# Optimization experiments

Hardware: AMD Instinct MI355X
Metric: run time of the kernel (lower is better)

## Reference

```python
import jax, jax.numpy as jnp
import numpy as np
from jax import lax

EPS = 1e-5

def _conv1d(x, w, b):
    # x: [B,C,L], w: [O,I,K], valid padding, stride 1
    y = lax.conv_general_dilated(x, w, window_strides=(1,), padding='VALID',
                                 dimension_numbers=('NCH', 'OIH', 'NCH'))
    return y + b[None, :, None]

def setup_inputs() -> dict:
    key = jax.random.key(0)
    ks = jax.random.split(key, 7)
    B, L, C = 16, 4096, 512
    x = jax.random.normal(ks[0], (B, L, C), dtype=jnp.float32)
    fan3 = 1.0 / np.sqrt(C * 3)
    fan1 = 1.0 / np.sqrt(C * 1)
    w_down = jax.random.uniform(ks[1], (C, C, 3), jnp.float32, -fan3, fan3)
    b_down = jax.random.uniform(ks[2], (C,), jnp.float32, -fan3, fan3)
    w_pad = jax.random.uniform(ks[3], (C, C, 1), jnp.float32, -fan1, fan1)
    b_pad = jax.random.uniform(ks[4], (C,), jnp.float32, -fan1, fan1)
    gamma = jnp.ones((C,), jnp.float32)
    beta = jnp.zeros((C,), jnp.float32)
    return {"x": x, "w_down": w_down, "b_down": b_down,
            "w_pad": w_pad, "b_pad": b_pad, "gamma": gamma, "beta": beta}

def reference(x, w_down, b_down, w_pad, b_pad, gamma, beta):
    # d == 2 branch of ConvLayer
    B, L, C = x.shape

    def branch(xs):  # xs: [B, L//2, C]
        xt = jnp.transpose(xs, (0, 2, 1))                 # [B,C,L/2]
        p1 = _conv1d(xt, w_down, b_down)                  # [B,C,L/2-2]
        p2 = _conv1d(xt[:, :, :2], w_pad, b_pad)          # [B,C,2]
        return jnp.concatenate([p1, p2], axis=2)          # [B,C,L/2]

    x1_p = branch(x[:, 0::2, :])
    x2_p = branch(x[:, 1::2, :])
    # interleave: even positions from x1_p, odd from x2_p
    x_p = jnp.stack([x1_p, x2_p], axis=3).reshape(B, C, L)

    # BatchNorm1d in training mode: batch stats over (batch, length)
    mean = jnp.mean(x_p, axis=(0, 2), keepdims=True)
    var = jnp.var(x_p, axis=(0, 2), keepdims=True)
    xn = (x_p - mean) * lax.rsqrt(var + EPS)
    xn = xn * gamma[None, :, None] + beta[None, :, None]

    y = jax.nn.elu(xn)                                    # dropout = identity (eval)
    y = y + jnp.transpose(x, (0, 2, 1))                   # residual [B,C,L]

    # MaxPool1d(kernel=3, stride=2, padding=1)
    yp = jnp.pad(y, ((0, 0), (0, 0), (1, 1)), constant_values=-jnp.inf)
    pooled = lax.reduce_window(yp, -jnp.inf, lax.max, (1, 1, 3), (1, 1, 2), 'VALID')
    return jnp.transpose(pooled, (0, 2, 1))               # [B, L//2, C]
```

## Files before the change

kernel.cpp:

```cpp
#include <hip/hip_runtime.h>
#include <hip/hip_bf16.h>
#include <math.h>

typedef __bf16 bf16;
typedef __bf16 bf16x8 __attribute__((ext_vector_type(8)));
typedef float floatx4 __attribute__((ext_vector_type(4)));

#define GAS __attribute__((address_space(1)))
#define LAS __attribute__((address_space(3)))

static constexpr int B_ = 16, L_ = 4096, C_ = 512;
static constexpr int M_ = B_ * L_;
static constexpr int K_ = 3 * C_;

__global__ void prep_w(const float* __restrict__ x,
                       const float* __restrict__ wd, bf16* __restrict__ wr,
                       const float* __restrict__ wp, const float* __restrict__ bp,
                       bf16* __restrict__ xp, float* __restrict__ sums) {
    __shared__ float xrow[C_];
    if (blockIdx.x < 512) {
        for (int u = blockIdx.x; u < 3072; u += 512) {
            int idx = u * 256 + threadIdx.x;
            int o   = idx / K_;
            int rem = idx - o * K_;
            int kk  = rem >> 9;
            int i   = rem & 511;
            wr[idx] = (bf16)wd[o * K_ + i * 3 + kk];
        }
    } else {
        const int bid = blockIdx.x - 512;
        const int b = bid >> 2;
        const int j = bid & 3;
        for (int i = threadIdx.x; i < C_; i += 256)
            xrow[i] = x[(size_t)(b * L_ + j) * C_ + i];
        __syncthreads();
        for (int c = threadIdx.x; c < C_; c += 256) {
            const float* w = wp + (size_t)c * C_;
            float acc = 0.f;
#pragma unroll 4
            for (int i = 0; i < C_; i += 4) {
                floatx4 wv = *(const floatx4*)(w + i);
#pragma unroll
                for (int u = 0; u < 4; ++u) acc += wv[u] * xrow[i + u];
            }
            const float v = acc + bp[c];
            xp[(size_t)(b * L_ + 4092 + j) * C_ + c] = (bf16)v;
            atomicAdd(&sums[c], v);
            atomicAdd(&sums[C_ + c], v * v);
        }
    }
}

__global__ __launch_bounds__(512, 2) void gemm_conv(
    const float* __restrict__ xf, const bf16* __restrict__ wr,
    const float* __restrict__ bd, bf16* __restrict__ xp,
    bf16* __restrict__ xb, float* __restrict__ sums)
{
    __shared__ bf16 As[2 * 256 * 64];
    __shared__ bf16 Bs[2 * 256 * 64];

    const int tid = threadIdx.x;
    const int u   = blockIdx.x;
    const int mb  = (u & 7) + 8 * (u >> 4);
    const int nb  = (u >> 3) & 1;
    const int m0  = mb * 256;
    const int n0  = nb * 256;

    const int wave = tid >> 6;
    const int lane = tid & 63;
    const int wm = wave & 1;
    const int wn = wave >> 1;
    const int tm = lane & 15;
    const int quad = lane >> 4;

    floatx4 acc[2][4][2][2];
#pragma unroll
    for (int a = 0; a < 2; ++a)
#pragma unroll
        for (int b = 0; b < 4; ++b)
#pragma unroll
            for (int c = 0; c < 2; ++c)
#pragma unroll
                for (int d = 0; d < 2; ++d) acc[a][b][c][d] = floatx4{0.f, 0.f, 0.f, 0.f};

    const int r0  = tid >> 3;
    const int c0s = (tid & 7) ^ (r0 & 7);

    auto issueA = [&](int ts, floatx4 (&va)[8]) {
        if (ts >= 24) return;
        const int kk = ts >> 3, i0 = (ts & 7) << 6;
#pragma unroll
        for (int eta = 0; eta < 2; ++eta) {
            int sr0 = m0 + eta * 128 + r0 + 2 * kk;      if (sr0 > M_ - 1) sr0 = M_ - 1;
            int sr1 = m0 + eta * 128 + r0 + 64 + 2 * kk; if (sr1 > M_ - 1) sr1 = M_ - 1;
            const float* p0 = xf + (size_t)sr0 * C_ + i0 + c0s * 8;
            const float* p1 = xf + (size_t)sr1 * C_ + i0 + c0s * 8;
            va[eta * 4 + 0] = *(const floatx4*)(p0);
            va[eta * 4 + 1] = *(const floatx4*)(p0 + 4);
            va[eta * 4 + 2] = *(const floatx4*)(p1);
            va[eta * 4 + 3] = *(const floatx4*)(p1 + 4);
        }
    };
    auto writeA = [&](int ts, const floatx4 (&va)[8]) {
        if (ts >= 24) return;
#pragma unroll
        for (int eta = 0; eta < 2; ++eta) {
            bf16* dst = As + (ts & 1) * 16384 + eta * 8192 + tid * 8;
            bf16x8 v0, v1;
#pragma unroll
            for (int j = 0; j < 4; ++j) {
                v0[j] = (bf16)va[eta * 4 + 0][j]; v0[4 + j] = (bf16)va[eta * 4 + 1][j];
                v1[j] = (bf16)va[eta * 4 + 2][j]; v1[4 + j] = (bf16)va[eta * 4 + 3][j];
            }
            *(bf16x8*)dst = v0;
            *(bf16x8*)(dst + 4096) = v1;
            if (nb == 0 && ts < 8) {
                const int i0 = ts << 6;
                const int sr0 = m0 + eta * 128 + r0;
                *(bf16x8*)(xb + (size_t)sr0 * C_ + i0 + c0s * 8) = v0;
                *(bf16x8*)(xb + (size_t)(sr0 + 64) * C_ + i0 + c0s * 8) = v1;
            }
        }
    };
    auto stageB = [&](int t, int eta) {
        if (t >= 24) return;
        const int kk = t >> 3, i0 = (t & 7) << 6;
        bf16* dst = Bs + (t & 1) * 16384 + eta * 8192 + tid * 8;
        const bf16* s0 = wr + (size_t)(n0 + eta * 128 + r0) * K_ + kk * C_ + i0 + c0s * 8;
        __builtin_amdgcn_global_load_lds((const GAS void*)s0, (LAS void*)dst, 16, 0, 0);
        __builtin_amdgcn_global_load_lds((const GAS void*)(s0 + (size_t)64 * K_),
                                         (LAS void*)(dst + 4096), 16, 0, 0);
    };

    const int xo0 = (quad ^ (tm & 7)) << 3;
    const int xo1 = ((4 + quad) ^ (tm & 7)) << 3;

    bf16x8 af[4][2];
    bf16x8 bfr[2][2][2];

    {
        floatx4 va0[8], va1[8];
        issueA(0, va0);
        issueA(1, va1);
        stageB(0, 0); stageB(0, 1); stageB(1, 0); stageB(1, 1);
        asm volatile("s_waitcnt vmcnt(8)" ::: "memory");
        writeA(0, va0);
        writeA(1, va1);
        asm volatile("s_waitcnt vmcnt(12) lgkmcnt(0)" ::: "memory");
        asm volatile("s_barrier" ::: "memory");
    }
#pragma unroll
    for (int mi = 0; mi < 4; ++mi) {
        const bf16* p = As + (wm * 64 + mi * 16 + tm) * 64;
        af[mi][0] = *(const bf16x8*)(p + xo0);
        af[mi][1] = *(const bf16x8*)(p + xo1);
    }
#pragma unroll
    for (int ni = 0; ni < 2; ++ni) {
        const bf16* p = Bs + (wn * 32 + ni * 16 + tm) * 64;
        bfr[0][ni][0] = *(const bf16x8*)(p + xo0);
        bfr[0][ni][1] = *(const bf16x8*)(p + xo1);
    }

#pragma unroll 2
    for (int t = 0; t < 24; ++t) {
        const bf16* Ab  = As + (t & 1) * 16384;
        const bf16* Bb  = Bs + (t & 1) * 16384;
        const bf16* AbN = As + ((t + 1) & 1) * 16384;
        const bf16* BbN = Bs + ((t + 1) & 1) * 16384;
        floatx4 va[8];

        asm volatile("s_waitcnt lgkmcnt(0)" ::: "memory");
        __builtin_amdgcn_sched_barrier(0);
        __builtin_amdgcn_s_setprio(1);
#pragma unroll
        for (int kh = 0; kh < 2; ++kh)
#pragma unroll
            for (int mi = 0; mi < 4; ++mi)
#pragma unroll
                for (int ni = 0; ni < 2; ++ni)
                    acc[0][mi][0][ni] = __builtin_amdgcn_mfma_f32_16x16x32_bf16(
                        af[mi][kh], bfr[0][ni][kh], acc[0][mi][0][ni], 0, 0, 0);
        __builtin_amdgcn_s_setprio(0);
#pragma unroll
        for (int ni = 0; ni < 2; ++ni) {
            const bf16* p = Bb + (128 + wn * 32 + ni * 16 + tm) * 64;
            bfr[1][ni][0] = *(const bf16x8*)(p + xo0);
            bfr[1][ni][1] = *(const bf16x8*)(p + xo1);
        }
        asm volatile("s_barrier" ::: "memory");

        asm volatile("s_waitcnt lgkmcnt(0)" ::: "memory");
        __builtin_amdgcn_sched_barrier(0);
        __builtin_amdgcn_s_setprio(1);
#pragma unroll
        for (int kh = 0; kh < 2; ++kh)
#pragma unroll
            for (int mi = 0; mi < 4; ++mi)
#pragma unroll
                for (int ni = 0; ni < 2; ++ni)
                    acc[0][mi][1][ni] = __builtin_amdgcn_mfma_f32_16x16x32_bf16(
                        af[mi][kh], bfr[1][ni][kh], acc[0][mi][1][ni], 0, 0, 0);
        __builtin_amdgcn_s_setprio(0);
#pragma unroll
        for (int mi = 0; mi < 4; ++mi) {
            const bf16* p = Ab + (128 + wm * 64 + mi * 16 + tm) * 64;
            af[mi][0] = *(const bf16x8*)(p + xo0);
            af[mi][1] = *(const bf16x8*)(p + xo1);
        }
        issueA(t + 2, va);
        stageB(t + 2, 0);
        asm volatile("s_barrier" ::: "memory");

        asm volatile("s_waitcnt lgkmcnt(0)" ::: "memory");
        __builtin_amdgcn_sched_barrier(0);
        __builtin_amdgcn_s_setprio(1);
#pragma unroll
        for (int kh = 0; kh < 2; ++kh)
#pragma unroll
            for (int mi = 0; mi < 4; ++mi)
#pragma unroll
                for (int ni = 0; ni < 2; ++ni)
                    acc[1][mi][1][ni] = __builtin_amdgcn_mfma_f32_16x16x32_bf16(
                        af[mi][kh], bfr[1][ni][kh], acc[1][mi][1][ni], 0, 0, 0);
        __builtin_amdgcn_s_setprio(0);
        stageB(t + 2, 1);
        asm volatile("s_barrier" ::: "memory");

        if (t < 22)       { asm volatile("s_waitcnt vmcnt(4)" ::: "memory"); }
        else if (t == 22) { asm volatile("s_waitcnt vmcnt(0)" ::: "memory"); }
        writeA(t + 2, va);
        asm volatile("s_barrier" ::: "memory");
        __builtin_amdgcn_s_setprio(1);
#pragma unroll
        for (int kh = 0; kh < 2; ++kh)
#pragma unroll
            for (int mi = 0; mi < 4; ++mi)
#pragma unroll
                for (int ni = 0; ni < 2; ++ni)
                    acc[1][mi][0][ni] = __builtin_amdgcn_mfma_f32_16x16x32_bf16(
                        af[mi][kh], bfr[0][ni][kh], acc[1][mi][0][ni], 0, 0, 0);
        __builtin_amdgcn_s_setprio(0);
        if (t < 23) {
#pragma unroll
            for (int mi = 0; mi < 4; ++mi) {
                const bf16* p = AbN + (wm * 64 + mi * 16 + tm) * 64;
                af[mi][0] = *(const bf16x8*)(p + xo0);
                af[mi][1] = *(const bf16x8*)(p + xo1);
            }
#pragma unroll
            for (int ni = 0; ni < 2; ++ni) {
                const bf16* p = BbN + (wn * 32 + ni * 16 + tm) * 64;
                bfr[0][ni][0] = *(const bf16x8*)(p + xo0);
                bfr[0][ni][1] = *(const bf16x8*)(p + xo1);
            }
        }
        asm volatile("s_barrier" ::: "memory");
    }

    float bias[2][2], s[2][2], q[2][2];
#pragma unroll
    for (int nh = 0; nh < 2; ++nh)
#pragma unroll
        for (int ni = 0; ni < 2; ++ni) {
            bias[nh][ni] = bd[n0 + nh * 128 + wn * 32 + ni * 16 + tm];
            s[nh][ni] = 0.f; q[nh][ni] = 0.f;
        }

#pragma unroll
    for (int mh = 0; mh < 2; ++mh)
#pragma unroll
        for (int mi = 0; mi < 4; ++mi)
#pragma unroll
            for (int r = 0; r < 4; ++r) {
                const int m = m0 + mh * 128 + wm * 64 + mi * 16 + quad * 4 + r;
                const bool valid = (m & (L_ - 1)) < L_ - 4;
                bf16* dst = xp + (size_t)m * C_ + n0 + wn * 32 + tm;
#pragma unroll
                for (int nh = 0; nh < 2; ++nh)
#pragma unroll
                    for (int ni = 0; ni < 2; ++ni) {
                        const float v = acc[mh][mi][nh][ni][r] + bias[nh][ni];
                        if (valid) {
                            dst[nh * 128 + ni * 16] = (bf16)v;
                            s[nh][ni] += v; q[nh][ni] += v * v;
                        }
                    }
            }
#pragma unroll
    for (int nh = 0; nh < 2; ++nh)
#pragma unroll
        for (int ni = 0; ni < 2; ++ni) {
            float sv = s[nh][ni], qv = q[nh][ni];
            sv += __shfl_xor(sv, 16); sv += __shfl_xor(sv, 32);
            qv += __shfl_xor(qv, 16); qv += __shfl_xor(qv, 32);
            if (quad == 0) {
                const int c = n0 + nh * 128 + wn * 32 + ni * 16 + tm;
                atomicAdd(&sums[c], sv);
                atomicAdd(&sums[C_ + c], qv);
            }
        }
}

__global__ void final_pool(const bf16* __restrict__ xp, const bf16* __restrict__ xb,
                           const float* __restrict__ sums, const float* __restrict__ gamma,
                           const float* __restrict__ beta, float* __restrict__ out)
{
    const int gid0 = blockIdx.x * 256 + threadIdx.x;
    const int cg = gid0 & 63;
    const int t  = (gid0 >> 6) & 2047;
    const int b0 = gid0 >> 17;
    const int c0 = cg << 3;

    float sc[8], sh[8];
    const float invn = 1.0f / 65536.0f;
#pragma unroll
    for (int j = 0; j < 8; ++j) {
        const int c = c0 + j;
        float mean = sums[c] * invn;
        float var  = sums[C_ + c] * invn - mean * mean;
        float scale = gamma[c] * rsqrtf(var + 1e-5f);
        sc[j] = scale;
        sh[j] = beta[c] - mean * scale;
    }

    for (int b = b0; b < B_; b += 4) {
        float best[8];
#pragma unroll
        for (int j = 0; j < 8; ++j) best[j] = -INFINITY;

#pragma unroll
        for (int dl = -1; dl <= 1; ++dl) {
            const int l = 2 * t + dl;
            if (l < 0) continue;
            const size_t off = (size_t)(b * L_ + l) * C_ + c0;
            bf16x8 xpv = *(const bf16x8*)(xp + off);
            bf16x8 xv  = *(const bf16x8*)(xb + off);
#pragma unroll
            for (int j = 0; j < 8; ++j) {
                float z = sc[j] * (float)xpv[j] + sh[j];
                float y = (z > 0.f) ? z : (__expf(z) - 1.f);
                y += (float)xv[j];
                best[j] = fmaxf(best[j], y);
            }
        }
        floatx4 o0, o1;
#pragma unroll
        for (int j = 0; j < 4; ++j) { o0[j] = best[j]; o1[j] = best[4 + j]; }
        const size_t og = ((size_t)b << 17) | ((size_t)t << 6) | cg;
        *(floatx4*)(out + og * 8) = o0;
        *(floatx4*)(out + og * 8 + 4) = o1;
    }
}

extern "C" void kernel_launch(void* const* d_in, const int* in_sizes, int n_in,
                              void* d_out, int out_size, void* d_ws, size_t ws_size,
                              hipStream_t stream)
{
    const float* x      = (const float*)d_in[0];
    const float* w_down = (const float*)d_in[1];
    const float* b_down = (const float*)d_in[2];
    const float* w_pad  = (const float*)d_in[3];
    const float* b_pad  = (const float*)d_in[4];
    const float* gamma  = (const float*)d_in[5];
    const float* beta   = (const float*)d_in[6];
    float* out = (float*)d_out;

    char* ws = (char*)d_ws;
    bf16*  xb   = (bf16*)ws;
    bf16*  xp   = (bf16*)(ws + (size_t)M_ * C_ * 2);
    bf16*  wr   = (bf16*)(ws + (size_t)M_ * C_ * 4);
    float* sums = (float*)(ws + (size_t)M_ * C_ * 4 + (size_t)C_ * K_ * 2);

    hipMemsetAsync(sums, 0, 2 * C_ * sizeof(float), stream);
    prep_w<<<dim3(512 + 64), dim3(256), 0, stream>>>(x, w_down, wr,
                                                     w_pad, b_pad, xp, sums);
    gemm_conv<<<dim3(512), dim3(512), 0, stream>>>(x, wr, b_down, xp, xb, sums);
    final_pool<<<dim3(2048), dim3(256), 0, stream>>>(xp, xb, sums, gamma, beta, out);
}
```

Measured before the change: 418.0 us.

## Drop bf16 residual copy; read fp32 x directly and pool two outputs per thread

The GEMM kernel no longer writes a bf16 copy of x for the residual, and the final pooling kernel reads the original fp32 x instead. The pooling kernel now computes two adjacent pooled outputs per thread from five input rows, so the overlapping middle row is loaded and its ELU computed once instead of twice. This removes the 64MB bf16 write and cuts redundant pooling reads, but the residual read doubles in width (fp32 vs bf16). The residual also becomes exact fp32 rather than bf16-rounded.

```diff
diff --git a/kernel.cpp b/kernel.cpp
--- a/kernel.cpp
+++ b/kernel.cpp
@@ -53,8 +53,7 @@
 
 __global__ __launch_bounds__(512, 2) void gemm_conv(
     const float* __restrict__ xf, const bf16* __restrict__ wr,
-    const float* __restrict__ bd, bf16* __restrict__ xp,
-    bf16* __restrict__ xb, float* __restrict__ sums)
+    const float* __restrict__ bd, bf16* __restrict__ xp, float* __restrict__ sums)
 {
     __shared__ bf16 As[2 * 256 * 64];
     __shared__ bf16 Bs[2 * 256 * 64];
@@ -114,12 +113,6 @@
             }
             *(bf16x8*)dst = v0;
             *(bf16x8*)(dst + 4096) = v1;
-            if (nb == 0 && ts < 8) {
-                const int i0 = ts << 6;
-                const int sr0 = m0 + eta * 128 + r0;
-                *(bf16x8*)(xb + (size_t)sr0 * C_ + i0 + c0s * 8) = v0;
-                *(bf16x8*)(xb + (size_t)(sr0 + 64) * C_ + i0 + c0s * 8) = v1;
-            }
         }
     };
     auto stageB = [&](int t, int eta) {
@@ -146,7 +139,7 @@
         asm volatile("s_waitcnt vmcnt(8)" ::: "memory");
         writeA(0, va0);
         writeA(1, va1);
-        asm volatile("s_waitcnt vmcnt(12) lgkmcnt(0)" ::: "memory");
+        asm volatile("s_waitcnt vmcnt(4) lgkmcnt(0)" ::: "memory");
         asm volatile("s_barrier" ::: "memory");
     }
 #pragma unroll
@@ -302,14 +295,14 @@
         }
 }
 
-__global__ void final_pool(const bf16* __restrict__ xp, const bf16* __restrict__ xb,
+__global__ void final_pool(const bf16* __restrict__ xp, const float* __restrict__ xf,
                            const float* __restrict__ sums, const float* __restrict__ gamma,
                            const float* __restrict__ beta, float* __restrict__ out)
 {
-    const int gid0 = blockIdx.x * 256 + threadIdx.x;
-    const int cg = gid0 & 63;
-    const int t  = (gid0 >> 6) & 2047;
-    const int b0 = gid0 >> 17;
+    const int gid = blockIdx.x * 256 + threadIdx.x;
+    const int cg = gid & 63;
+    const int tp = (gid >> 6) & 1023;
+    const int b0 = gid >> 16;
     const int c0 = cg << 3;
 
     float sc[8], sh[8];
@@ -324,32 +317,40 @@
         sh[j] = beta[c] - mean * scale;
     }
 
-    for (int b = b0; b < B_; b += 4) {
-        float best[8];
-#pragma unroll
-        for (int j = 0; j < 8; ++j) best[j] = -INFINITY;
-
-#pragma unroll
-        for (int dl = -1; dl <= 1; ++dl) {
-            const int l = 2 * t + dl;
-            if (l < 0) continue;
+    for (int b = b0; b < B_; b += 8) {
+        float y[5][8];
+#pragma unroll
+        for (int i = 0; i < 5; ++i) {
+            const int l = 4 * tp - 1 + i;
+            if (l < 0) {
+#pragma unroll
+                for (int j = 0; j < 8; ++j) y[i][j] = -INFINITY;
+                continue;
+            }
             const size_t off = (size_t)(b * L_ + l) * C_ + c0;
             bf16x8 xpv = *(const bf16x8*)(xp + off);
-            bf16x8 xv  = *(const bf16x8*)(xb + off);
+            floatx4 xa = *(const floatx4*)(xf + off);
+            floatx4 xbv = *(const floatx4*)(xf + off + 4);
 #pragma unroll
             for (int j = 0; j < 8; ++j) {
                 float z = sc[j] * (float)xpv[j] + sh[j];
-                float y = (z > 0.f) ? z : (__expf(z) - 1.f);
-                y += (float)xv[j];
-                best[j] = fmaxf(best[j], y);
-            }
-        }
-        floatx4 o0, o1;
-#pragma unroll
-        for (int j = 0; j < 4; ++j) { o0[j] = best[j]; o1[j] = best[4 + j]; }
-        const size_t og = ((size_t)b << 17) | ((size_t)t << 6) | cg;
-        *(floatx4*)(out + og * 8) = o0;
-        *(floatx4*)(out + og * 8 + 4) = o1;
+                float e = (z > 0.f) ? z : (__expf(z) - 1.f);
+                y[i][j] = e + (j < 4 ? xa[j] : xbv[j - 4]);
+            }
+        }
+        floatx4 o0a, o0b, o1a, o1b;
+#pragma unroll
+        for (int j = 0; j < 4; ++j) {
+            o0a[j] = fmaxf(fmaxf(y[0][j], y[1][j]), y[2][j]);
+            o0b[j] = fmaxf(fmaxf(y[0][4 + j], y[1][4 + j]), y[2][4 + j]);
+            o1a[j] = fmaxf(fmaxf(y[2][j], y[3][j]), y[4][j]);
+            o1b[j] = fmaxf(fmaxf(y[2][4 + j], y[3][4 + j]), y[4][4 + j]);
+        }
+        const size_t og0 = ((size_t)b * 2048 + 2 * tp) * C_ + c0;
+        *(floatx4*)(out + og0) = o0a;
+        *(floatx4*)(out + og0 + 4) = o0b;
+        *(floatx4*)(out + og0 + C_) = o1a;
+        *(floatx4*)(out + og0 + C_ + 4) = o1b;
     }
 }
 
@@ -367,14 +368,13 @@
     float* out = (float*)d_out;
 
     char* ws = (char*)d_ws;
-    bf16*  xb   = (bf16*)ws;
-    bf16*  xp   = (bf16*)(ws + (size_t)M_ * C_ * 2);
-    bf16*  wr   = (bf16*)(ws + (size_t)M_ * C_ * 4);
-    float* sums = (float*)(ws + (size_t)M_ * C_ * 4 + (size_t)C_ * K_ * 2);
+    bf16*  xp   = (bf16*)ws;
+    bf16*  wr   = (bf16*)(ws + (size_t)M_ * C_ * 2);
+    float* sums = (float*)(ws + (size_t)M_ * C_ * 2 + (size_t)C_ * K_ * 2);
 
     hipMemsetAsync(sums, 0, 2 * C_ * sizeof(float), stream);
     prep_w<<<dim3(512 + 64), dim3(256), 0, stream>>>(x, w_down, wr,
                                                      w_pad, b_pad, xp, sums);
-    gemm_conv<<<dim3(512), dim3(512), 0, stream>>>(x, wr, b_down, xp, xb, sums);
-    final_pool<<<dim3(2048), dim3(256), 0, stream>>>(xp, xb, sums, gamma, beta, out);
+    gemm_conv<<<dim3(512), dim3(512), 0, stream>>>(x, wr, b_down, xp, sums);
+    final_pool<<<dim3(2048), dim3(256), 0, stream>>>(xp, x, sums, gamma, beta, out);
 }
```

New measurement: 408.7 us. 2.2% less time.
